# Optimization experiments

Measured on AMD Instinct MI355X. Metric: run time of the kernel, lower is better.

The kernel has to match this reference:

```python
import jax, jax.numpy as jnp
import numpy as np

NUM_CAMS = 1
NUM_HEADS = 1
NUM_LEVELS = 1
NUM_POINTS = 4
NUM_DEPTH = 128
EMBED = 128  # must equal NUM_DEPTH (output_proj is applied to the depth axis)


def setup_inputs() -> dict:
    key0 = jax.random.key(0)
    ks = jax.random.split(key0, 12)
    bsv, nq, nv = 1, 1024, 1024  # nq == nv == H*W (32*32)
    off_dim = NUM_CAMS * NUM_HEADS * NUM_LEVELS * NUM_DEPTH * NUM_POINTS * 2  # 1024
    aw_dim = NUM_CAMS * NUM_HEADS * NUM_LEVELS * NUM_DEPTH * NUM_POINTS       # 512
    return {
        "query": jax.random.normal(ks[0], (bsv, nq, EMBED), jnp.float32),
        "key": jax.random.normal(ks[1], (NUM_CAMS, nv, bsv, EMBED), jnp.float32),
        "value": jax.random.normal(ks[2], (NUM_CAMS, nv, bsv, EMBED), jnp.float32),
        "ref_3d": jax.random.uniform(ks[3], (bsv * NUM_CAMS, nq * NUM_DEPTH, 2), jnp.float32),
        "spatial_shapes": jnp.array([[32, 32]], dtype=jnp.int32),
        "W_off": jax.random.normal(ks[4], (EMBED, off_dim), jnp.float32) * 0.02,
        "b_off": jax.random.normal(ks[5], (off_dim,), jnp.float32) * 0.02,
        "W_attn": jax.random.normal(ks[6], (EMBED, aw_dim), jnp.float32) * 0.02,
        "b_attn": jax.random.normal(ks[7], (aw_dim,), jnp.float32) * 0.02,
        "W_v": jax.random.normal(ks[8], (EMBED, EMBED), jnp.float32) / np.sqrt(EMBED),
        "b_v": jnp.zeros((EMBED,), jnp.float32),
        "W_o": jax.random.normal(ks[9], (EMBED, EMBED), jnp.float32) / np.sqrt(EMBED),
        "b_o": jnp.zeros((EMBED,), jnp.float32),
    }


def _bilinear_sample(val, H, W, x, y):
    """grid_sample(align_corners=False, padding=zeros) equivalent.
    val: [B, H*W, D]; x, y: [B, Q, P] in pixel coords. Returns [B, Q, P, D]."""
    B, Q, P = x.shape
    D = val.shape[-1]
    x0f = jnp.floor(x); y0f = jnp.floor(y)
    ix0 = x0f.astype(jnp.int32); iy0 = y0f.astype(jnp.int32)
    wx1 = x - x0f; wy1 = y - y0f
    wx0 = 1.0 - wx1; wy0 = 1.0 - wy1

    def corner(ix, iy, w):
        valid = (ix >= 0) & (ix < W) & (iy >= 0) & (iy < H)
        idx = jnp.clip(iy, 0, H - 1) * W + jnp.clip(ix, 0, W - 1)  # [B,Q,P]
        g = jnp.take_along_axis(val, idx.reshape(B, Q * P)[:, :, None], axis=1)
        g = g.reshape(B, Q, P, D)
        return g * (w * valid.astype(val.dtype))[..., None]

    return (corner(ix0, iy0, wx0 * wy0)
            + corner(ix0 + 1, iy0, wx1 * wy0)
            + corner(ix0, iy0 + 1, wx0 * wy1)
            + corner(ix0 + 1, iy0 + 1, wx1 * wy1))


def reference(query, key, value, ref_3d, spatial_shapes,
              W_off, b_off, W_attn, b_attn, W_v, b_v, W_o, b_o):
    bsv, nq, E = query.shape
    cams, nv, bs, _ = key.shape
    identity = query

    # key/value: [cams, nv, bs, E] -> [bsv, nv, E]
    key2 = jnp.transpose(key, (2, 0, 1, 3)).reshape(bsv, nv, E)
    val = jnp.flip(value, axis=0)
    val = jnp.transpose(val, (2, 0, 1, 3)).reshape(bsv, nv, E)
    val = val @ W_v + b_v
    val = val.reshape(bsv * cams, nv, E)  # num_heads=1 -> head_dim=E

    # offsets / attention weights (heads=levels=1 axes squeezed)
    off = (query @ W_off + b_off).reshape(bsv, nq, cams, NUM_DEPTH, NUM_POINTS, 2)
    aw = (query @ W_attn + b_attn).reshape(bsv, nq, cams, NUM_DEPTH, NUM_LEVELS * NUM_POINTS)
    aw = jax.nn.softmax(aw, axis=-1).reshape(bsv, nq, cams, NUM_DEPTH, NUM_POINTS)
    off = jnp.transpose(off, (0, 2, 1, 3, 4, 5)).reshape(bsv * cams, nq * NUM_DEPTH, NUM_POINTS, 2)
    aw = jnp.transpose(aw, (0, 2, 1, 3, 4)).reshape(bsv * cams, nq * NUM_DEPTH, NUM_POINTS)

    H = spatial_shapes[0, 0]
    W = spatial_shapes[0, 1]
    norm = jnp.stack([W, H]).astype(off.dtype)  # [W, H]
    loc = ref_3d[:, :, None, :] + off / norm    # [B, Qe, P, 2] in [0,1]
    x = loc[..., 0] * W.astype(loc.dtype) - 0.5
    y = loc[..., 1] * H.astype(loc.dtype) - 0.5

    sampled = _bilinear_sample(val, H, W, x, y)          # [B, Qe, P, E]
    out = jnp.einsum('bqpe,bqp->bqe', sampled, aw)       # weighted sum over points

    out = out.reshape(bsv, cams, nq, NUM_DEPTH, E).mean(axis=1)  # [bsv, nq, depth, E]
    out = (out * key2[:, :, None, :]).mean(axis=-1)              # [bsv, nq, depth]
    out = out @ W_o + b_o                                        # depth == EMBED
    return out + identity  # dropout = identity in eval
```

## Files before the change

kernel.cpp:

```cpp
#include <hip/hip_runtime.h>


#define NQ   1024
#define NV   1024
#define ND   128
#define NP   4
#define IMG_W 32
#define IMG_H 32
#define QB   4

typedef __attribute__((ext_vector_type(8))) short bfx8;
typedef __attribute__((ext_vector_type(4))) float f32x4;

__device__ __forceinline__ unsigned short bf_rne(float f) {
  unsigned u = __float_as_uint(f);
  return (unsigned short)((u + 0x7FFFu + ((u >> 16) & 1u)) >> 16);
}

__global__ __launch_bounds__(256) void mono_kernel(
    const float* __restrict__ query, const float* __restrict__ key,
    const float* __restrict__ value, const float* __restrict__ ref3d,
    const float* __restrict__ W_off, const float* __restrict__ b_off,
    const float* __restrict__ W_attn, const float* __restrict__ b_attn,
    const float* __restrict__ W_v, const float* __restrict__ b_v,
    const float* __restrict__ W_o, const float* __restrict__ b_o,
    float* __restrict__ out) {
  __shared__ float q_lds[QB][128];
  __shared__ float img[QB][NV];
  __shared__ float off_lds[QB][1024];
  __shared__ float aw_lds[QB][512];
  __shared__ float c_lds[QB];
  __shared__ __align__(16) char Ru[16384];
  float* key_lds  = (float*)Ru;
  float* keyp_lds = (float*)(Ru + 2048);
  unsigned short* sval = (unsigned short*)Ru;
  float* o1s = (float*)Ru;

  const int tid = threadIdx.x;
  const int q0 = blockIdx.x * QB;
  const int w = tid >> 6, l = tid & 63;

  if (tid < 128) {
    ((float4*)q_lds)[tid] = ((const float4*)(query + (size_t)q0 * 128))[tid];
  } else {
    ((float4*)key_lds)[tid - 128] =
        ((const float4*)(key + (size_t)q0 * 128))[tid - 128];
  }
  __syncthreads();

  {
    float4 aoff[QB];
    float2 aaw[QB];
#pragma unroll
    for (int qq = 0; qq < QB; ++qq) {
      aoff[qq] = make_float4(0.f, 0.f, 0.f, 0.f);
      aaw[qq] = make_float2(0.f, 0.f);
    }
    const float* wo_p = W_off + (size_t)tid * 4;
    const float* wa_p = W_attn + (size_t)tid * 2;
#pragma unroll 4
    for (int e4 = 0; e4 < 32; ++e4) {
      float4 q4[QB];
#pragma unroll
      for (int qq = 0; qq < QB; ++qq)
        q4[qq] = *(const float4*)(&q_lds[qq][e4 * 4]);
#pragma unroll
      for (int j = 0; j < 4; ++j) {
        const int e = e4 * 4 + j;
        const float4 w4 = *(const float4*)(wo_p + (size_t)e * 1024);
        const float2 w2 = *(const float2*)(wa_p + (size_t)e * 512);
#pragma unroll
        for (int qq = 0; qq < QB; ++qq) {
          const float* qp = (const float*)&q4[qq];
          const float qv = qp[j];
          aoff[qq].x = fmaf(qv, w4.x, aoff[qq].x);
          aoff[qq].y = fmaf(qv, w4.y, aoff[qq].y);
          aoff[qq].z = fmaf(qv, w4.z, aoff[qq].z);
          aoff[qq].w = fmaf(qv, w4.w, aoff[qq].w);
          aaw[qq].x = fmaf(qv, w2.x, aaw[qq].x);
          aaw[qq].y = fmaf(qv, w2.y, aaw[qq].y);
        }
      }
    }
    const float4 bo4 = *(const float4*)(b_off + tid * 4);
    const float2 ba2 = *(const float2*)(b_attn + tid * 2);
#pragma unroll
    for (int qq = 0; qq < QB; ++qq) {
      float4 r;
      r.x = aoff[qq].x + bo4.x; r.y = aoff[qq].y + bo4.y;
      r.z = aoff[qq].z + bo4.z; r.w = aoff[qq].w + bo4.w;
      *(float4*)(&off_lds[qq][tid * 4]) = r;
      float2 r2;
      r2.x = aaw[qq].x + ba2.x; r2.y = aaw[qq].y + ba2.y;
      *(float2*)(&aw_lds[qq][tid * 2]) = r2;
    }
  }

  {
    const int h = l >> 5, e4s = l & 31;
#pragma unroll 2
    for (int s = 0; s < 16; ++s) {
      const int i = w * 32 + s * 2 + h;
      const float4 wv = *(const float4*)(W_v + (size_t)i * 128 + e4s * 4);
      float p[QB];
#pragma unroll
      for (int qq = 0; qq < QB; ++qq) {
        const float4 k4 = *(const float4*)(key_lds + qq * 128 + e4s * 4);
        p[qq] = fmaf(wv.x, k4.x,
                fmaf(wv.y, k4.y, fmaf(wv.z, k4.z, wv.w * k4.w)));
      }
#pragma unroll
      for (int m = 1; m < 32; m <<= 1)
#pragma unroll
        for (int qq = 0; qq < QB; ++qq) p[qq] += __shfl_xor(p[qq], m);
      if (e4s == 0)
#pragma unroll
        for (int qq = 0; qq < QB; ++qq) keyp_lds[qq * 128 + i] = p[qq];
    }
    if (tid < QB) {
      float s = 0.f;
      for (int e = 0; e < 128; e += 4) {
        const float4 bv = *(const float4*)(b_v + e);
        const float4 k4 = *(const float4*)(key_lds + tid * 128 + e);
        s = fmaf(bv.x, k4.x,
            fmaf(bv.y, k4.y, fmaf(bv.z, k4.z, fmaf(bv.w, k4.w, s))));
      }
      c_lds[tid] = s;
    }
  }
  __syncthreads();

  bfx8 afrag[4];
  {
    const int row = l & 15, g = l >> 4;
#pragma unroll
    for (int ks = 0; ks < 4; ++ks) {
      bfx8 a;
      if (row < QB) {
        const float* kp = keyp_lds + row * 128 + ks * 32 + g * 8;
#pragma unroll
        for (int j = 0; j < 8; ++j) a[j] = (short)bf_rne(kp[j]);
      } else {
#pragma unroll
        for (int j = 0; j < 8; ++j) a[j] = 0;
      }
      afrag[ks] = a;
    }
  }
  __syncthreads();

  for (int vt = 0; vt < 16; ++vt) {
#pragma unroll
    for (int it = 0; it < 4; ++it) {
      const int c = tid + it * 256;
      const int r = c >> 4, cc = c & 15;
      const float* p = value + (size_t)(vt * 64 + r) * 128 + cc * 8;
      const float4 f0 = *(const float4*)p;
      const float4 f1 = *(const float4*)(p + 4);
      bfx8 vv;
      vv[0] = (short)bf_rne(f0.x); vv[1] = (short)bf_rne(f0.y);
      vv[2] = (short)bf_rne(f0.z); vv[3] = (short)bf_rne(f0.w);
      vv[4] = (short)bf_rne(f1.x); vv[5] = (short)bf_rne(f1.y);
      vv[6] = (short)bf_rne(f1.z); vv[7] = (short)bf_rne(f1.w);
      const int byte = r * 256 + ((cc * 16) ^ ((r & 15) << 4));
      *(bfx8*)((char*)sval + byte) = vv;
    }
    __syncthreads();

    {
      const int col = l & 15, g = l >> 4;
      const int r = w * 16 + col;
      f32x4 acc = {0.f, 0.f, 0.f, 0.f};
#pragma unroll
      for (int ks = 0; ks < 4; ++ks) {
        const int colb = (ks * 64 + g * 16) ^ (col << 4);
        const bfx8 bfr = *(const bfx8*)((const char*)sval + r * 256 + colb);
        acc = __builtin_amdgcn_mfma_f32_16x16x32_bf16(afrag[ks], bfr, acc,
                                                      0, 0, 0);
      }
      if (g == 0) {
        const int v = vt * 64 + w * 16 + col;
#pragma unroll
        for (int i = 0; i < QB; ++i) img[i][v] = acc[i] + c_lds[i];
      }
    }
    __syncthreads();
  }

#pragma unroll
  for (int pass = 0; pass < 2; ++pass) {
    const int qq = (tid >> 7) + 2 * pass;
    const int q = q0 + qq;
    const int d = tid & 127;
    const float* im = img[qq];
    const size_t qe = (size_t)q * ND + d;

    const float rx = ref3d[qe * 2 + 0];
    const float ry = ref3d[qe * 2 + 1];

    const float* awp = &aw_lds[qq][d * NP];
    const float a0 = awp[0], a1 = awp[1], a2 = awp[2], a3 = awp[3];
    const float mx = fmaxf(fmaxf(a0, a1), fmaxf(a2, a3));
    const float e0 = __expf(a0 - mx), e1 = __expf(a1 - mx),
                e2 = __expf(a2 - mx), e3 = __expf(a3 - mx);
    const float inv = 1.0f / (e0 + e1 + e2 + e3);
    const float wgt4[4] = {e0 * inv, e1 * inv, e2 * inv, e3 * inv};

    const float* op = &off_lds[qq][d * (NP * 2)];

    float acc = 0.0f;
#pragma unroll
    for (int p = 0; p < NP; ++p) {
      const float x = rx * (float)IMG_W + op[p * 2 + 0] - 0.5f;
      const float y = ry * (float)IMG_H + op[p * 2 + 1] - 0.5f;
      const float xf = floorf(x), yf = floorf(y);
      const int ix0 = (int)xf, iy0 = (int)yf;
      const float wx1 = x - xf, wy1 = y - yf;
      const float wx0 = 1.0f - wx1, wy0 = 1.0f - wy1;

      float s = 0.0f;
#pragma unroll
      for (int cy = 0; cy < 2; ++cy) {
#pragma unroll
        for (int cx = 0; cx < 2; ++cx) {
          const int ix = ix0 + cx, iy = iy0 + cy;
          const bool valid = (ix >= 0) & (ix < IMG_W) & (iy >= 0) & (iy < IMG_H);
          const int cix = min(max(ix, 0), IMG_W - 1);
          const int ciy = min(max(iy, 0), IMG_H - 1);
          const float wgt = (cx ? wx1 : wx0) * (cy ? wy1 : wy0);
          s += valid ? im[ciy * IMG_W + cix] * wgt : 0.0f;
        }
      }
      acc += wgt4[p] * s;
    }
    o1s[qq * ND + d] = acc * (1.0f / 128.0f);
  }
  __syncthreads();

  {
    const int qqA = tid >> 7, qqB = qqA + 2;
    const int n = tid & 127;
    float acc0 = b_o[n] + q_lds[qqA][n];
    float acc1 = b_o[n] + q_lds[qqB][n];
#pragma unroll 8
    for (int d = 0; d < 128; ++d) {
      const float wv = W_o[(size_t)d * 128 + n];
      acc0 = fmaf(o1s[qqA * ND + d], wv, acc0);
      acc1 = fmaf(o1s[qqB * ND + d], wv, acc1);
    }
    out[(size_t)(q0 + qqA) * 128 + n] = acc0;
    out[(size_t)(q0 + qqB) * 128 + n] = acc1;
  }
}

extern "C" void kernel_launch(void* const* d_in, const int* in_sizes, int n_in,
                              void* d_out, int out_size, void* d_ws, size_t ws_size,
                              hipStream_t stream) {
  const float* query  = (const float*)d_in[0];
  const float* key    = (const float*)d_in[1];
  const float* value  = (const float*)d_in[2];
  const float* ref3d  = (const float*)d_in[3];
  const float* W_off  = (const float*)d_in[5];
  const float* b_off  = (const float*)d_in[6];
  const float* W_attn = (const float*)d_in[7];
  const float* b_attn = (const float*)d_in[8];
  const float* W_v    = (const float*)d_in[9];
  const float* b_v    = (const float*)d_in[10];
  const float* W_o    = (const float*)d_in[11];
  const float* b_o    = (const float*)d_in[12];
  float* out = (float*)d_out;

  mono_kernel<<<NQ / QB, 256, 0, stream>>>(query, key, value, ref3d,
                                           W_off, b_off, W_attn, b_attn,
                                           W_v, b_v, W_o, b_o, out);
}
```

Measured before the change: 119.4 us.

## Double block size, store intermediates as bf16, and compute key projection with MFMA

Raises the block to 512 threads so each thread handles fewer offset/attention columns and one query row in the sampling and output stages. The value tile per iteration grows to 128 rows, halving the loop trips. The key projection through W_v moves from a shuffle reduction to a bf16 MFMA over a staged W_v tile. The image, offsets and attention logits are stored in LDS as bf16 to fit the larger shared footprint. This adds rounding error to the sampling coordinates and logits, and the larger LDS use may limit how many blocks fit per CU.

```diff
diff --git a/kernel.cpp b/kernel.cpp
--- a/kernel.cpp
+++ b/kernel.cpp
@@ -16,8 +16,18 @@
   unsigned u = __float_as_uint(f);
   return (unsigned short)((u + 0x7FFFu + ((u >> 16) & 1u)) >> 16);
 }
-
-__global__ __launch_bounds__(256) void mono_kernel(
+__device__ __forceinline__ float bf2f(unsigned short u) {
+  return __uint_as_float((unsigned)u << 16);
+}
+
+__device__ __forceinline__ bfx8 pack8(const float* p) {
+  bfx8 v;
+#pragma unroll
+  for (int j = 0; j < 8; ++j) v[j] = (short)bf_rne(p[j]);
+  return v;
+}
+
+__global__ __launch_bounds__(512) void mono_kernel(
     const float* __restrict__ query, const float* __restrict__ key,
     const float* __restrict__ value, const float* __restrict__ ref3d,
     const float* __restrict__ W_off, const float* __restrict__ b_off,
@@ -26,15 +36,14 @@
     const float* __restrict__ W_o, const float* __restrict__ b_o,
     float* __restrict__ out) {
   __shared__ float q_lds[QB][128];
-  __shared__ float img[QB][NV];
-  __shared__ float off_lds[QB][1024];
-  __shared__ float aw_lds[QB][512];
+  __shared__ float key_lds[QB][128];
+  __shared__ float keyp_lds[QB][128];
   __shared__ float c_lds[QB];
-  __shared__ __align__(16) char Ru[16384];
-  float* key_lds  = (float*)Ru;
-  float* keyp_lds = (float*)(Ru + 2048);
-  unsigned short* sval = (unsigned short*)Ru;
-  float* o1s = (float*)Ru;
+  __shared__ unsigned short img_bf[QB][NV];
+  __shared__ unsigned short off_bf[QB][1024];
+  __shared__ unsigned short aw_bf[QB][512];
+  __shared__ __align__(16) unsigned short sval[128 * 128];
+  float* o1s = (float*)sval;
 
   const int tid = threadIdx.x;
   const int q0 = blockIdx.x * QB;
@@ -42,22 +51,22 @@
 
   if (tid < 128) {
     ((float4*)q_lds)[tid] = ((const float4*)(query + (size_t)q0 * 128))[tid];
-  } else {
+  } else if (tid < 256) {
     ((float4*)key_lds)[tid - 128] =
         ((const float4*)(key + (size_t)q0 * 128))[tid - 128];
   }
   __syncthreads();
 
   {
-    float4 aoff[QB];
-    float2 aaw[QB];
+    float2 aoff[QB];
+    float aaw[QB];
 #pragma unroll
     for (int qq = 0; qq < QB; ++qq) {
-      aoff[qq] = make_float4(0.f, 0.f, 0.f, 0.f);
-      aaw[qq] = make_float2(0.f, 0.f);
-    }
-    const float* wo_p = W_off + (size_t)tid * 4;
-    const float* wa_p = W_attn + (size_t)tid * 2;
+      aoff[qq] = make_float2(0.f, 0.f);
+      aaw[qq] = 0.f;
+    }
+    const float* wo_p = W_off + (size_t)tid * 2;
+    const float* wa_p = W_attn + tid;
 #pragma unroll 4
     for (int e4 = 0; e4 < 32; ++e4) {
       float4 q4[QB];
@@ -67,61 +76,76 @@
 #pragma unroll
       for (int j = 0; j < 4; ++j) {
         const int e = e4 * 4 + j;
-        const float4 w4 = *(const float4*)(wo_p + (size_t)e * 1024);
-        const float2 w2 = *(const float2*)(wa_p + (size_t)e * 512);
+        const float2 w2 = *(const float2*)(wo_p + (size_t)e * 1024);
+        const float wa = wa_p[(size_t)e * 512];
 #pragma unroll
         for (int qq = 0; qq < QB; ++qq) {
           const float* qp = (const float*)&q4[qq];
           const float qv = qp[j];
-          aoff[qq].x = fmaf(qv, w4.x, aoff[qq].x);
-          aoff[qq].y = fmaf(qv, w4.y, aoff[qq].y);
-          aoff[qq].z = fmaf(qv, w4.z, aoff[qq].z);
-          aoff[qq].w = fmaf(qv, w4.w, aoff[qq].w);
-          aaw[qq].x = fmaf(qv, w2.x, aaw[qq].x);
-          aaw[qq].y = fmaf(qv, w2.y, aaw[qq].y);
+          aoff[qq].x = fmaf(qv, w2.x, aoff[qq].x);
+          aoff[qq].y = fmaf(qv, w2.y, aoff[qq].y);
+          aaw[qq] = fmaf(qv, wa, aaw[qq]);
         }
       }
     }
-    const float4 bo4 = *(const float4*)(b_off + tid * 4);
-    const float2 ba2 = *(const float2*)(b_attn + tid * 2);
+    const float2 bo2 = *(const float2*)(b_off + tid * 2);
+    const float ba = b_attn[tid];
 #pragma unroll
     for (int qq = 0; qq < QB; ++qq) {
-      float4 r;
-      r.x = aoff[qq].x + bo4.x; r.y = aoff[qq].y + bo4.y;
-      r.z = aoff[qq].z + bo4.z; r.w = aoff[qq].w + bo4.w;
-      *(float4*)(&off_lds[qq][tid * 4]) = r;
-      float2 r2;
-      r2.x = aaw[qq].x + ba2.x; r2.y = aaw[qq].y + ba2.y;
-      *(float2*)(&aw_lds[qq][tid * 2]) = r2;
-    }
-  }
-
-  {
-    const int h = l >> 5, e4s = l & 31;
-#pragma unroll 2
-    for (int s = 0; s < 16; ++s) {
-      const int i = w * 32 + s * 2 + h;
-      const float4 wv = *(const float4*)(W_v + (size_t)i * 128 + e4s * 4);
-      float p[QB];
-#pragma unroll
-      for (int qq = 0; qq < QB; ++qq) {
-        const float4 k4 = *(const float4*)(key_lds + qq * 128 + e4s * 4);
-        p[qq] = fmaf(wv.x, k4.x,
-                fmaf(wv.y, k4.y, fmaf(wv.z, k4.z, wv.w * k4.w)));
-      }
-#pragma unroll
-      for (int m = 1; m < 32; m <<= 1)
-#pragma unroll
-        for (int qq = 0; qq < QB; ++qq) p[qq] += __shfl_xor(p[qq], m);
-      if (e4s == 0)
-#pragma unroll
-        for (int qq = 0; qq < QB; ++qq) keyp_lds[qq * 128 + i] = p[qq];
+      const unsigned px = (unsigned)bf_rne(aoff[qq].x + bo2.x) |
+                          ((unsigned)bf_rne(aoff[qq].y + bo2.y) << 16);
+      *(unsigned*)(&off_bf[qq][tid * 2]) = px;
+      aw_bf[qq][tid] = bf_rne(aaw[qq] + ba);
+    }
+  }
+
+  {
+#pragma unroll
+    for (int it = 0; it < 4; ++it) {
+      const int c = tid + it * 512;
+      const int r = c >> 4, cc = c & 15;
+      const bfx8 v = pack8(W_v + (size_t)r * 128 + cc * 8);
+      const int byte = r * 256 + ((cc * 16) ^ ((r & 15) << 4));
+      *(bfx8*)((char*)sval + byte) = v;
+    }
+    bfx8 afK[4];
+    {
+      const int row = l & 15, g = l >> 4;
+#pragma unroll
+      for (int ks = 0; ks < 4; ++ks) {
+        bfx8 a;
+        if (row < QB) {
+          a = pack8(&key_lds[row][ks * 32 + g * 8]);
+        } else {
+#pragma unroll
+          for (int j = 0; j < 8; ++j) a[j] = 0;
+        }
+        afK[ks] = a;
+      }
+    }
+    __syncthreads();
+
+    {
+      const int col = l & 15, g = l >> 4;
+      const int r = w * 16 + col;
+      f32x4 acc = {0.f, 0.f, 0.f, 0.f};
+#pragma unroll
+      for (int ks = 0; ks < 4; ++ks) {
+        const int colb = (ks * 64 + g * 16) ^ (col << 4);
+        const bfx8 bfr = *(const bfx8*)((const char*)sval + r * 256 + colb);
+        acc = __builtin_amdgcn_mfma_f32_16x16x32_bf16(afK[ks], bfr, acc,
+                                                      0, 0, 0);
+      }
+      if (g == 0) {
+#pragma unroll
+        for (int i = 0; i < QB; ++i) keyp_lds[i][r] = acc[i];
+      }
     }
     if (tid < QB) {
       float s = 0.f;
       for (int e = 0; e < 128; e += 4) {
         const float4 bv = *(const float4*)(b_v + e);
-        const float4 k4 = *(const float4*)(key_lds + tid * 128 + e);
+        const float4 k4 = *(const float4*)(&key_lds[tid][e]);
         s = fmaf(bv.x, k4.x,
             fmaf(bv.y, k4.y, fmaf(bv.z, k4.z, fmaf(bv.w, k4.w, s))));
       }
@@ -137,9 +161,7 @@
     for (int ks = 0; ks < 4; ++ks) {
       bfx8 a;
       if (row < QB) {
-        const float* kp = keyp_lds + row * 128 + ks * 32 + g * 8;
-#pragma unroll
-        for (int j = 0; j < 8; ++j) a[j] = (short)bf_rne(kp[j]);
+        a = pack8(&keyp_lds[row][ks * 32 + g * 8]);
       } else {
 #pragma unroll
         for (int j = 0; j < 8; ++j) a[j] = 0;
@@ -149,21 +171,14 @@
   }
   __syncthreads();
 
-  for (int vt = 0; vt < 16; ++vt) {
+  for (int vt = 0; vt < 8; ++vt) {
 #pragma unroll
     for (int it = 0; it < 4; ++it) {
-      const int c = tid + it * 256;
+      const int c = tid + it * 512;
       const int r = c >> 4, cc = c & 15;
-      const float* p = value + (size_t)(vt * 64 + r) * 128 + cc * 8;
-      const float4 f0 = *(const float4*)p;
-      const float4 f1 = *(const float4*)(p + 4);
-      bfx8 vv;
-      vv[0] = (short)bf_rne(f0.x); vv[1] = (short)bf_rne(f0.y);
-      vv[2] = (short)bf_rne(f0.z); vv[3] = (short)bf_rne(f0.w);
-      vv[4] = (short)bf_rne(f1.x); vv[5] = (short)bf_rne(f1.y);
-      vv[6] = (short)bf_rne(f1.z); vv[7] = (short)bf_rne(f1.w);
+      const bfx8 v = pack8(value + (size_t)(vt * 128 + r) * 128 + cc * 8);
       const int byte = r * 256 + ((cc * 16) ^ ((r & 15) << 4));
-      *(bfx8*)((char*)sval + byte) = vv;
+      *(bfx8*)((char*)sval + byte) = v;
     }
     __syncthreads();
 
@@ -179,40 +194,44 @@
                                                       0, 0, 0);
       }
       if (g == 0) {
-        const int v = vt * 64 + w * 16 + col;
-#pragma unroll
-        for (int i = 0; i < QB; ++i) img[i][v] = acc[i] + c_lds[i];
-      }
-    }
-    __syncthreads();
-  }
-
-#pragma unroll
-  for (int pass = 0; pass < 2; ++pass) {
-    const int qq = (tid >> 7) + 2 * pass;
+        const int v = vt * 128 + r;
+#pragma unroll
+        for (int i = 0; i < QB; ++i)
+          img_bf[i][v] = bf_rne(acc[i] + c_lds[i]);
+      }
+    }
+    __syncthreads();
+  }
+
+  {
+    const int qq = tid >> 7;
     const int q = q0 + qq;
     const int d = tid & 127;
-    const float* im = img[qq];
+    const unsigned short* im = img_bf[qq];
     const size_t qe = (size_t)q * ND + d;
 
     const float rx = ref3d[qe * 2 + 0];
     const float ry = ref3d[qe * 2 + 1];
 
-    const float* awp = &aw_lds[qq][d * NP];
-    const float a0 = awp[0], a1 = awp[1], a2 = awp[2], a3 = awp[3];
+    const uint2 ua = *(const uint2*)(&aw_bf[qq][d * 4]);
+    const float a0 = bf2f((unsigned short)(ua.x & 0xffff));
+    const float a1 = bf2f((unsigned short)(ua.x >> 16));
+    const float a2 = bf2f((unsigned short)(ua.y & 0xffff));
+    const float a3 = bf2f((unsigned short)(ua.y >> 16));
     const float mx = fmaxf(fmaxf(a0, a1), fmaxf(a2, a3));
     const float e0 = __expf(a0 - mx), e1 = __expf(a1 - mx),
                 e2 = __expf(a2 - mx), e3 = __expf(a3 - mx);
     const float inv = 1.0f / (e0 + e1 + e2 + e3);
     const float wgt4[4] = {e0 * inv, e1 * inv, e2 * inv, e3 * inv};
 
-    const float* op = &off_lds[qq][d * (NP * 2)];
+    const uint4 uo = *(const uint4*)(&off_bf[qq][d * 8]);
+    const unsigned ox[4] = {uo.x, uo.y, uo.z, uo.w};
 
     float acc = 0.0f;
 #pragma unroll
     for (int p = 0; p < NP; ++p) {
-      const float x = rx * (float)IMG_W + op[p * 2 + 0] - 0.5f;
-      const float y = ry * (float)IMG_H + op[p * 2 + 1] - 0.5f;
+      const float x = rx * (float)IMG_W + bf2f((unsigned short)(ox[p] & 0xffff)) - 0.5f;
+      const float y = ry * (float)IMG_H + bf2f((unsigned short)(ox[p] >> 16)) - 0.5f;
       const float xf = floorf(x), yf = floorf(y);
       const int ix0 = (int)xf, iy0 = (int)yf;
       const float wx1 = x - xf, wy1 = y - yf;
@@ -228,28 +247,24 @@
           const int cix = min(max(ix, 0), IMG_W - 1);
           const int ciy = min(max(iy, 0), IMG_H - 1);
           const float wgt = (cx ? wx1 : wx0) * (cy ? wy1 : wy0);
-          s += valid ? im[ciy * IMG_W + cix] * wgt : 0.0f;
+          s += valid ? bf2f(im[ciy * IMG_W + cix]) * wgt : 0.0f;
         }
       }
       acc += wgt4[p] * s;
     }
+    __syncthreads();
     o1s[qq * ND + d] = acc * (1.0f / 128.0f);
   }
   __syncthreads();
 
   {
-    const int qqA = tid >> 7, qqB = qqA + 2;
+    const int qq = tid >> 7;
     const int n = tid & 127;
-    float acc0 = b_o[n] + q_lds[qqA][n];
-    float acc1 = b_o[n] + q_lds[qqB][n];
+    float acc = b_o[n] + q_lds[qq][n];
 #pragma unroll 8
-    for (int d = 0; d < 128; ++d) {
-      const float wv = W_o[(size_t)d * 128 + n];
-      acc0 = fmaf(o1s[qqA * ND + d], wv, acc0);
-      acc1 = fmaf(o1s[qqB * ND + d], wv, acc1);
-    }
-    out[(size_t)(q0 + qqA) * 128 + n] = acc0;
-    out[(size_t)(q0 + qqB) * 128 + n] = acc1;
+    for (int d = 0; d < 128; ++d)
+      acc = fmaf(o1s[qq * ND + d], W_o[(size_t)d * 128 + n], acc);
+    out[(size_t)(q0 + qq) * 128 + n] = acc;
   }
 }
 
@@ -270,7 +285,7 @@
   const float* b_o    = (const float*)d_in[12];
   float* out = (float*)d_out;
 
-  mono_kernel<<<NQ / QB, 256, 0, stream>>>(query, key, value, ref3d,
+  mono_kernel<<<NQ / QB, 512, 0, stream>>>(query, key, value, ref3d,
                                            W_off, b_off, W_attn, b_attn,
                                            W_v, b_v, W_o, b_o, out);
 }
```

After: 108.2 us. 1.1x faster.
